# Kernel optimization log

Hardware: AMD Instinct MI355X
Metric: run time of the kernel (lower is better)

Reference implementation:

```python
import jax, jax.numpy as jnp
import numpy as np

T_SEG = 8      # n_segment
KSZ = 3        # LAM temporal kernel size
PAD = 1        # LAM temporal padding
BN_EPS = 1e-5


def setup_inputs() -> dict:
    key = jax.random.key(0)
    ks = jax.random.split(key, 12)
    n, t, c, h, w = 8, T_SEG, 256, 56, 56
    return {
        "x": jax.random.normal(ks[0], (n * t, c, h, w), jnp.float32),
        "net_w": jax.random.normal(ks[1], (c, c, 3, 3), jnp.float32) * 0.02,
        "net_b": jax.random.normal(ks[2], (c,), jnp.float32) * 0.02,
        "lam_w": jax.random.normal(ks[3], (c, c), jnp.float32) * 0.02,
        "lam_b": jax.random.normal(ks[4], (c,), jnp.float32) * 0.02,
        "mlp_w1": jax.random.normal(ks[5], (2 * t, t), jnp.float32) * 0.3,
        "bn_gamma": jax.random.uniform(ks[6], (2 * t,), jnp.float32, 0.5, 1.5),
        "bn_beta": jax.random.normal(ks[7], (2 * t,), jnp.float32) * 0.1,
        "bn_mean": jax.random.normal(ks[8], (2 * t,), jnp.float32) * 0.1,
        "bn_var": jax.random.uniform(ks[9], (2 * t,), jnp.float32, 0.5, 1.5),
        "mlp_w2": jax.random.normal(ks[10], (KSZ, 2 * t), jnp.float32) * 0.3,
        "me_w": jax.random.normal(ks[11], (3,), jnp.float32) * 0.3,
    }


def reference(x, net_w, net_b, lam_w, lam_b, mlp_w1, bn_gamma, bn_beta,
              bn_mean, bn_var, mlp_w2, me_w):
    t = T_SEG
    nt, c, h, w = x.shape
    n = nt // t

    # --- wrapped net: Conv2d 3x3, pad 1 ---
    out = jax.lax.conv_general_dilated(
        x, net_w, window_strides=(1, 1), padding="SAME",
        dimension_numbers=("NCHW", "OIHW", "NCHW"))
    out = out + net_b[None, :, None, None]

    # --- LAM ---
    new_x = out.reshape(n, t, c, h, w).transpose(0, 2, 1, 3, 4)  # (n,c,t,h,w)
    x_g = new_x.mean(axis=(2, 3, 4))                   # global pool -> (n,c)
    x_g = x_g @ lam_w.T + lam_b                        # Conv1d k=1 == matmul
    new_x = new_x + x_g[:, :, None, None, None]

    pooled = new_x.mean(axis=(3, 4)).reshape(n * c, t)  # per-(n,c) temporal sig
    hdn = pooled @ mlp_w1.T                              # (n*c, 2t), no bias
    hdn = (hdn - bn_mean) * (bn_gamma / jnp.sqrt(bn_var + BN_EPS)) + bn_beta
    hdn = jax.nn.relu(hdn)
    wgt = jax.nn.softmax(hdn @ mlp_w2.T, axis=-1).reshape(n, c, KSZ)

    # grouped conv2d (groups=n*c) == per-(n,c) depthwise temporal conv
    xpad = jnp.pad(new_x, ((0, 0), (0, 0), (PAD, PAD), (0, 0), (0, 0)))
    lam_out = sum(wgt[:, :, k, None, None, None] * xpad[:, :, k:k + t]
                  for k in range(KSZ))                  # (n,c,t,h,w)
    lam_out = lam_out.transpose(0, 2, 1, 3, 4).reshape(nt, c, h, w)

    # --- ME ---
    xv = lam_out.reshape(n, t, c, h, w)
    diff = xv[:, 1:] - xv[:, :-1]                       # frame differences
    diff = jnp.pad(diff, ((0, 0), (0, 1), (0, 0), (0, 0), (0, 0)))
    diff = diff.reshape(nt, c, h, w)
    y = diff.mean(axis=(2, 3))                          # (nt, c)
    ypad = jnp.pad(y, ((0, 0), (1, 1)))                 # conv1d over channel dim
    yc = sum(me_w[k] * ypad[:, k:k + c] for k in range(3))
    gate = jax.nn.sigmoid(yc)[:, :, None, None]

    return gate * lam_out
```

## Files before the change

kernel.cpp:

```cpp
#include <hip/hip_runtime.h>
#include <hip/hip_bf16.h>
#include <stdint.h>

#define AS1 __attribute__((address_space(1)))
#define AS3 __attribute__((address_space(3)))

typedef __attribute__((ext_vector_type(8))) short short8v;
typedef __attribute__((ext_vector_type(4))) unsigned short ushort4v;
typedef __attribute__((ext_vector_type(4))) float float4v;

#define NT 64
#define CCH 256
#define HH 56
#define WW 56
#define HWSZ 3136
#define HP 58
#define WP 58

#define OFF_XT   0ull
#define SZ_XT    110231552ull
#define OFF_WPK  (OFF_XT + SZ_XT)
#define SZ_WPK   1179648ull
#define OFF_CS   (OFF_WPK + SZ_WPK)
#define SZ_CS    65536ull
#define OFF_XG2  (OFF_CS + SZ_CS)
#define SZ_XG2   8192ull
#define OFF_WGT  (OFF_XG2 + SZ_XG2)
#define SZ_WGT   24576ull
#define OFF_GATE (OFF_WGT + SZ_WGT)
#define SZ_GATE  65536ull
#define OFF_CVT  (OFF_GATE + SZ_GATE)
#define SZ_CVT   102760448ull

__device__ __forceinline__ unsigned short f2bf(float f) {
    unsigned int u = __float_as_uint(f);
    unsigned int r = (u + 0x7fffu + ((u >> 16) & 1u)) >> 16;
    return (unsigned short)r;
}
__device__ __forceinline__ float bf2f(unsigned short u) {
    return __uint_as_float(((unsigned int)u) << 16);
}

__device__ __forceinline__ void gload16(const unsigned short* g, unsigned short* l) {
    __builtin_amdgcn_global_load_lds((const AS1 void*)g, (AS3 void*)l, 16, 0, 0);
}

__global__ __launch_bounds__(256) void k0_transpose(const float* __restrict__ x,
                                                    unsigned short* __restrict__ xt) {
    int b = blockIdx.x;
    int cb = b & 3;
    int h  = (b >> 2) % 56;
    int nt = b / (4 * 56);
    int c0 = cb * 64;
    int tid = threadIdx.x;

    __shared__ float xs[64 * 57];

    const float* src = x + ((size_t)nt * CCH + c0) * HWSZ + h * WW;
    for (int li = tid; li < 896; li += 256) {
        int row = li / 14, f4 = li % 14;
        float4v v = *(const float4v*)(src + (size_t)row * HWSZ + f4 * 4);
        float* d = &xs[row * 57 + f4 * 4];
        d[0] = v.x; d[1] = v.y; d[2] = v.z; d[3] = v.w;
    }
    __syncthreads();

    unsigned short* dst = xt + (((size_t)nt * HP + (h + 1)) * WP) * CCH + c0;
    for (int job = tid; job < 464; job += 256) {
        int ww = job >> 3, cg = job & 7;
        short8v v;
        if (ww == 0 || ww == 57) {
            v = (short8v){0,0,0,0,0,0,0,0};
        } else {
            #pragma unroll
            for (int jj = 0; jj < 8; ++jj)
                v[jj] = (short)f2bf(xs[(cg * 8 + jj) * 57 + (ww - 1)]);
        }
        *(short8v*)(dst + ww * CCH + cg * 8) = v;
    }
    if (h == 0) {
        unsigned short* d0  = xt + ((size_t)nt * HP + 0)  * WP * CCH + c0;
        unsigned short* d57 = xt + ((size_t)nt * HP + 57) * WP * CCH + c0;
        short8v z = (short8v){0,0,0,0,0,0,0,0};
        for (int job = tid; job < 464; job += 256) {
            int ww = job >> 3, cg = job & 7;
            *(short8v*)(d0  + ww * CCH + cg * 8) = z;
            *(short8v*)(d57 + ww * CCH + cg * 8) = z;
        }
    }
}

__global__ __launch_bounds__(256) void kw_pack(const float* __restrict__ nw,
                                               unsigned short* __restrict__ wpk) {
    int idx = blockIdx.x * 256 + threadIdx.x;
    int rs = idx >> 16;
    int k  = (idx >> 8) & 255;
    int c  = idx & 255;
    wpk[idx] = f2bf(nw[(k * 256 + c) * 9 + rs]);
}


#define STGALL(bi_, tA_, tB_) do { \
    gload16(wpk + (tA_) + aoffg0, &lds[(bi_) * 8192 + ldsa0]); \
    gload16(wpk + (tA_) + aoffg1, &lds[(bi_) * 8192 + ldsa1]); \
    gload16(xt  + (tB_) + boffg,  &lds[24576 + (bi_) * 4096 + ldsb]); \
} while (0)

#define LDAF(mi) (*(const short8v*)&lds[abase + (wm * 64 + (mi) * 16 + r16) * 32 + pA * 8])
#define LDBF(j)  (*(const short8v*)&lds[bbase + (wp * 64 + (j) * 16 + r16) * 32 + pA * 8])

#define BARSYNC do { \
    __builtin_amdgcn_s_barrier(); \
    __builtin_amdgcn_sched_barrier(0); \
} while (0)

template <int OB>
__global__ __launch_bounds__(512, 4) void conv_mfma(const unsigned short* __restrict__ xt,
                                                    const unsigned short* __restrict__ wpk,
                                                    const float* __restrict__ net_b,
                                                    float* __restrict__ out,
                                                    unsigned short* __restrict__ cvt,
                                                    float* __restrict__ chansum) {
    __shared__ unsigned short lds[36864];

    const int tid  = threadIdx.x;
    const int lane = tid & 63;
    const int wid  = tid >> 6;
    const int wm   = wid >> 1;
    const int wp   = wid & 1;
    const int r16  = lane & 15;
    const int hi   = lane >> 4;
    const int pA   = (hi + (r16 >> 1)) & 3;

    const int pb0 = (blockIdx.x & 7) * 192 + (blockIdx.x >> 3);

    const int cgs = ((tid & 3) - (tid >> 3)) & 3;
    const int aoffg0 = (tid >> 2) * 256 + cgs * 8;
    const int aoffg1 = aoffg0 + 32768;
    const int ldsa0  = tid * 8;
    const int ldsa1  = ldsa0 + 4096;
    const int ldsb   = tid * 8;

    for (int g = pb0; g < 1568; g += 1536) {
        const int p0 = g * 128;

        long boffg;
        {
            int r = tid >> 2;
            int p = p0 + r;
            int nt = p / HWSZ, hw = p - nt * HWSZ;
            int hh = hw / WW,  w  = hw - hh * WW;
            boffg = ((long)(nt * HP + hh) * WP + w) * 256 + cgs * 8;
        }

        float4v acc[4][4];
        #pragma unroll
        for (int i = 0; i < 4; ++i)
            #pragma unroll
            for (int j = 0; j < 4; ++j) acc[i][j] = (float4v){0.f, 0.f, 0.f, 0.f};

        STGALL(0, 0, 0);
        STGALL(1, 32, 32);

        int cur = 0;
        for (int kt = 0; kt < 72; ++kt) {
            const int abase = cur * 8192;
            const int bbase = 24576 + cur * 4096;

            if (kt < 70) {
                const int ktn = kt + 2;
                int nb2 = cur + 2; if (nb2 >= 3) nb2 -= 3;
                const int rsn = ktn >> 3, con = (ktn & 7) * 32;
                const int tAn = rsn * 65536 + con;
                const int tBn = ((rsn / 3) * WP + (rsn - (rsn / 3) * 3)) * 256 + con;
                STGALL(nb2, tAn, tBn);
                asm volatile("s_waitcnt vmcnt(6)" ::: "memory");
            } else if (kt == 70) {
                asm volatile("s_waitcnt vmcnt(3)" ::: "memory");
            } else {
                asm volatile("s_waitcnt vmcnt(0)" ::: "memory");
            }
            BARSYNC;

            short8v afrag[4], bfrag[4];
            #pragma unroll
            for (int mi = 0; mi < 4; ++mi) afrag[mi] = LDAF(mi);
            #pragma unroll
            for (int j = 0; j < 4; ++j) bfrag[j] = LDBF(j);

            asm volatile("s_waitcnt lgkmcnt(0)" ::: "memory");
            __builtin_amdgcn_sched_barrier(0);
            __builtin_amdgcn_s_setprio(1);
            #pragma unroll
            for (int j = 0; j < 4; ++j)
                #pragma unroll
                for (int mi = 0; mi < 4; ++mi)
                    acc[mi][j] = __builtin_amdgcn_mfma_f32_16x16x32_bf16(afrag[mi], bfrag[j], acc[mi][j], 0, 0, 0);
            __builtin_amdgcn_s_setprio(0);
            BARSYNC;

            ++cur; if (cur >= 3) cur = 0;
        }

        const int pw = p0 + wp * 64;
        const int ntw = pw / HWSZ;
        const int hwb = pw - ntw * HWSZ;
        #pragma unroll
        for (int mi = 0; mi < 4; ++mi) {
            #pragma unroll
            for (int r = 0; r < 4; ++r) {
                const int m = wm * 64 + mi * 16 + hi * 4 + r;
                const float bias = net_b[m];
                float csum = 0.f;
                const size_t obase = ((size_t)ntw * CCH + m) * HWSZ + hwb;
                #pragma unroll
                for (int j = 0; j < 4; ++j) {
                    float v = acc[mi][j][r] + bias;
                    if (OB) cvt[obase + j * 16 + r16] = f2bf(v);
                    else    out[obase + j * 16 + r16] = v;
                    csum += v;
                }
                csum += __shfl_xor(csum, 1);
                csum += __shfl_xor(csum, 2);
                csum += __shfl_xor(csum, 4);
                csum += __shfl_xor(csum, 8);
                if (r16 == 0) atomicAdd(&chansum[ntw * CCH + m], csum);
            }
        }
    }
}

__global__ __launch_bounds__(256) void k234(const float* __restrict__ chansum,
                                            const float* __restrict__ lam_w,
                                            const float* __restrict__ lam_b,
                                            const float* __restrict__ mw1,
                                            const float* __restrict__ bg,
                                            const float* __restrict__ bb,
                                            const float* __restrict__ bm,
                                            const float* __restrict__ bv,
                                            const float* __restrict__ mw2,
                                            const float* __restrict__ me_w,
                                            float* __restrict__ xg2,
                                            float* __restrict__ wgt,
                                            float* __restrict__ gate) {
    int n = blockIdx.x, c = threadIdx.x;
    __shared__ float xs[256];
    __shared__ float yd[8][256];

    float s = 0.f;
    #pragma unroll
    for (int t = 0; t < 8; ++t) s += chansum[(n * 8 + t) * CCH + c];
    xs[c] = s * (1.0f / (3136.f * 8.f));
    __syncthreads();

    float xg = lam_b[c];
    const float* row = lam_w + c * 256;
    for (int cc = 0; cc < 256; ++cc) xg += row[cc] * xs[cc];
    xg2[n * 256 + c] = xg;

    float p[8];
    #pragma unroll
    for (int t = 0; t < 8; ++t)
        p[t] = chansum[(n * 8 + t) * CCH + c] * (1.0f / 3136.f) + xg;

    float hd[16];
    #pragma unroll
    for (int j = 0; j < 16; ++j) {
        float v = 0.f;
        #pragma unroll
        for (int t = 0; t < 8; ++t) v += p[t] * mw1[j * 8 + t];
        v = (v - bm[j]) * (bg[j] * rsqrtf(bv[j] + 1e-5f)) + bb[j];
        hd[j] = fmaxf(v, 0.f);
    }
    float lg[3];
    #pragma unroll
    for (int k = 0; k < 3; ++k) {
        float v = 0.f;
        #pragma unroll
        for (int j = 0; j < 16; ++j) v += hd[j] * mw2[k * 16 + j];
        lg[k] = v;
    }
    float mx = fmaxf(fmaxf(lg[0], lg[1]), lg[2]);
    float e0 = expf(lg[0] - mx), e1 = expf(lg[1] - mx), e2 = expf(lg[2] - mx);
    float inv = 1.f / (e0 + e1 + e2);
    float wk[3] = {e0 * inv, e1 * inv, e2 * inv};
    int idx = n * 256 + c;
    #pragma unroll
    for (int k = 0; k < 3; ++k) wgt[idx * 3 + k] = wk[k];

    float mb[8];
    #pragma unroll
    for (int t = 0; t < 8; ++t) {
        float v = 0.f;
        #pragma unroll
        for (int k = 0; k < 3; ++k) {
            int tt = t + k - 1;
            if (tt >= 0 && tt < 8) v += wk[k] * p[tt];
        }
        mb[t] = v;
    }
    #pragma unroll
    for (int t = 0; t < 7; ++t) yd[t][c] = mb[t + 1] - mb[t];
    yd[7][c] = 0.f;
    __syncthreads();

    float w0 = me_w[0], w1v = me_w[1], w2v = me_w[2];
    #pragma unroll
    for (int t = 0; t < 8; ++t) {
        float yc = w1v * yd[t][c];
        if (c > 0)   yc += w0 * yd[t][c - 1];
        if (c < 255) yc += w2v * yd[t][c + 1];
        gate[(n * 8 + t) * CCH + c] = 1.f / (1.f + expf(-yc));
    }
}

template <int OB>
__global__ __launch_bounds__(256) void k5_final(float* __restrict__ out,
                                                const unsigned short* __restrict__ cvt,
                                                const float* __restrict__ wgt,
                                                const float* __restrict__ xg2,
                                                const float* __restrict__ gate) {
    int tid = blockIdx.x * 256 + threadIdx.x;
    int hw4 = tid % 784;
    int nc = tid / 784;
    int n = nc >> 8, c = nc & 255;
    float w0 = wgt[nc * 3 + 0], w1 = wgt[nc * 3 + 1], w2 = wgt[nc * 3 + 2];
    float xg = xg2[nc];
    const size_t tstride = (size_t)CCH * HWSZ;
    size_t base = ((size_t)(n * 8) * CCH + c) * HWSZ + hw4 * 4;

    float4v o[8];
    #pragma unroll
    for (int t = 0; t < 8; ++t) {
        if (OB) {
            ushort4v v = *(const ushort4v*)(cvt + base + t * tstride);
            #pragma unroll
            for (int q = 0; q < 4; ++q) o[t][q] = bf2f(v[q]);
        } else {
            o[t] = *(const float4v*)(out + base + t * tstride);
        }
    }

    #pragma unroll
    for (int t = 0; t < 8; ++t) {
        float g = gate[(n * 8 + t) * CCH + c];
        float4v lam;
        #pragma unroll
        for (int q = 0; q < 4; ++q) {
            float v = w1 * (o[t][q] + xg);
            if (t > 0) v += w0 * (o[t - 1][q] + xg);
            if (t < 7) v += w2 * (o[t + 1][q] + xg);
            lam[q] = g * v;
        }
        *(float4v*)(out + base + t * tstride) = lam;
    }
}

extern "C" void kernel_launch(void* const* d_in, const int* in_sizes, int n_in,
                              void* d_out, int out_size, void* d_ws, size_t ws_size,
                              hipStream_t stream) {
    const float* x      = (const float*)d_in[0];
    const float* net_w  = (const float*)d_in[1];
    const float* net_b  = (const float*)d_in[2];
    const float* lam_w  = (const float*)d_in[3];
    const float* lam_b  = (const float*)d_in[4];
    const float* mlp_w1 = (const float*)d_in[5];
    const float* bn_g   = (const float*)d_in[6];
    const float* bn_b   = (const float*)d_in[7];
    const float* bn_m   = (const float*)d_in[8];
    const float* bn_v   = (const float*)d_in[9];
    const float* mlp_w2 = (const float*)d_in[10];
    const float* me_w   = (const float*)d_in[11];
    float* out = (float*)d_out;

    char* ws = (char*)d_ws;
    unsigned short* xt  = (unsigned short*)(ws + OFF_XT);
    unsigned short* wpk = (unsigned short*)(ws + OFF_WPK);
    float* chansum = (float*)(ws + OFF_CS);
    float* xg2     = (float*)(ws + OFF_XG2);
    float* wgt     = (float*)(ws + OFF_WGT);
    float* gate    = (float*)(ws + OFF_GATE);
    unsigned short* cvt = (unsigned short*)(ws + OFF_CVT);

    const bool use_bf16 = (ws_size >= OFF_CVT + SZ_CVT);

    hipMemsetAsync(chansum, 0, SZ_CS, stream);
    kw_pack<<<2304, 256, 0, stream>>>(net_w, wpk);
    k0_transpose<<<64 * 56 * 4, 256, 0, stream>>>(x, xt);
    if (use_bf16)
        conv_mfma<1><<<1536, 512, 0, stream>>>(xt, wpk, net_b, out, cvt, chansum);
    else
        conv_mfma<0><<<1536, 512, 0, stream>>>(xt, wpk, net_b, out, cvt, chansum);
    k234<<<8, 256, 0, stream>>>(chansum, lam_w, lam_b, mlp_w1, bn_g, bn_b, bn_m, bn_v,
                                mlp_w2, me_w, xg2, wgt, gate);
    if (use_bf16)
        k5_final<1><<<6272, 256, 0, stream>>>(out, cvt, wgt, xg2, gate);
    else
        k5_final<0><<<6272, 256, 0, stream>>>(out, cvt, wgt, xg2, gate);
}
```

Baseline: 412.5 us.

## Split tail conv tiles along K across extra blocks with atomic accumulation

The conv GEMM has 1568 pixel tiles but launched 1536 blocks, so 32 blocks ran a second full tile serially, creating a long tail. The tail 32 tiles are now split into two K-halves each, handled by 64 extra blocks that atomically add partial results into a bias-preinitialized fp32 output. A new init kernel writes the bias into the tail region and the bias contribution into the channel sums, and the final kernel reads tail pixels from fp32 instead of bf16. This adds an extra kernel launch and float atomics on the output in exchange for removing the serialized second wave.

```diff
diff --git a/kernel.cpp b/kernel.cpp
--- a/kernel.cpp
+++ b/kernel.cpp
@@ -16,6 +16,7 @@
 #define HWSZ 3136
 #define HP 58
 #define WP 58
+#define TAILP 196608
 
 #define OFF_XT   0ull
 #define SZ_XT    110231552ull
@@ -99,6 +100,23 @@
     wpk[idx] = f2bf(nw[(k * 256 + c) * 9 + rs]);
 }
 
+__global__ __launch_bounds__(256) void kinit(const float* __restrict__ net_b,
+                                             float* __restrict__ out,
+                                             float* __restrict__ chansum) {
+    int idx = blockIdx.x * 256 + threadIdx.x;
+    int m  = idx >> 12;
+    int pp = idx & 4095;
+    int p  = TAILP + pp;
+    int nt = p / HWSZ, hw = p - nt * HWSZ;
+    out[((size_t)nt * CCH + m) * HWSZ + hw] = net_b[m];
+    if (pp < 512) {
+        int img = 62 + (pp >> 8);
+        int mm  = pp & 255;
+        float npix = (img == 62) ? 960.f : 3136.f;
+        chansum[img * CCH + mm] = npix * net_b[mm];
+    }
+}
+
 
 #define STGALL(bi_, tA_, tB_) do { \
     gload16(wpk + (tA_) + aoffg0, &lds[(bi_) * 8192 + ldsa0]); \
@@ -109,10 +127,30 @@
 #define LDAF(mi) (*(const short8v*)&lds[abase + (wm * 64 + (mi) * 16 + r16) * 32 + pA * 8])
 #define LDBF(j)  (*(const short8v*)&lds[bbase + (wp * 64 + (j) * 16 + r16) * 32 + pA * 8])
 
+#define KTA(kt) ((((kt) >> 3) << 16) + (((kt) & 7) * 32))
+#define KTB(kt) (((((kt) >> 3) / 3) * WP + (((kt) >> 3) - (((kt) >> 3) / 3) * 3)) * 256 + (((kt) & 7) * 32))
+
 #define BARSYNC do { \
     __builtin_amdgcn_s_barrier(); \
     __builtin_amdgcn_sched_barrier(0); \
 } while (0)
+
+#define KTILE_BODY \
+    short8v afrag[4], bfrag[4]; \
+    _Pragma("unroll") \
+    for (int mi = 0; mi < 4; ++mi) afrag[mi] = LDAF(mi); \
+    _Pragma("unroll") \
+    for (int j = 0; j < 4; ++j) bfrag[j] = LDBF(j); \
+    asm volatile("s_waitcnt lgkmcnt(0)" ::: "memory"); \
+    __builtin_amdgcn_sched_barrier(0); \
+    __builtin_amdgcn_s_setprio(1); \
+    _Pragma("unroll") \
+    for (int j = 0; j < 4; ++j) \
+        _Pragma("unroll") \
+        for (int mi = 0; mi < 4; ++mi) \
+            acc[mi][j] = __builtin_amdgcn_mfma_f32_16x16x32_bf16(afrag[mi], bfrag[j], acc[mi][j], 0, 0, 0); \
+    __builtin_amdgcn_s_setprio(0); \
+    BARSYNC;
 
 template <int OB>
 __global__ __launch_bounds__(512, 4) void conv_mfma(const unsigned short* __restrict__ xt,
@@ -132,7 +170,7 @@
     const int hi   = lane >> 4;
     const int pA   = (hi + (r16 >> 1)) & 3;
 
-    const int pb0 = (blockIdx.x & 7) * 192 + (blockIdx.x >> 3);
+    const int bid = blockIdx.x;
 
     const int cgs = ((tid & 3) - (tid >> 3)) & 3;
     const int aoffg0 = (tid >> 2) * 256 + cgs * 8;
@@ -141,8 +179,15 @@
     const int ldsa1  = ldsa0 + 4096;
     const int ldsb   = tid * 8;
 
-    for (int g = pb0; g < 1568; g += 1536) {
-        const int p0 = g * 128;
+    float4v acc[4][4];
+    #pragma unroll
+    for (int i = 0; i < 4; ++i)
+        #pragma unroll
+        for (int j = 0; j < 4; ++j) acc[i][j] = (float4v){0.f, 0.f, 0.f, 0.f};
+
+    if (bid < 1536) {
+        const int pb0 = (bid & 7) * 192 + (bid >> 3);
+        const int p0 = pb0 * 128;
 
         long boffg;
         {
@@ -153,12 +198,6 @@
             boffg = ((long)(nt * HP + hh) * WP + w) * 256 + cgs * 8;
         }
 
-        float4v acc[4][4];
-        #pragma unroll
-        for (int i = 0; i < 4; ++i)
-            #pragma unroll
-            for (int j = 0; j < 4; ++j) acc[i][j] = (float4v){0.f, 0.f, 0.f, 0.f};
-
         STGALL(0, 0, 0);
         STGALL(1, 32, 32);
 
@@ -170,10 +209,7 @@
             if (kt < 70) {
                 const int ktn = kt + 2;
                 int nb2 = cur + 2; if (nb2 >= 3) nb2 -= 3;
-                const int rsn = ktn >> 3, con = (ktn & 7) * 32;
-                const int tAn = rsn * 65536 + con;
-                const int tBn = ((rsn / 3) * WP + (rsn - (rsn / 3) * 3)) * 256 + con;
-                STGALL(nb2, tAn, tBn);
+                STGALL(nb2, KTA(ktn), KTB(ktn));
                 asm volatile("s_waitcnt vmcnt(6)" ::: "memory");
             } else if (kt == 70) {
                 asm volatile("s_waitcnt vmcnt(3)" ::: "memory");
@@ -182,23 +218,7 @@
             }
             BARSYNC;
 
-            short8v afrag[4], bfrag[4];
-            #pragma unroll
-            for (int mi = 0; mi < 4; ++mi) afrag[mi] = LDAF(mi);
-            #pragma unroll
-            for (int j = 0; j < 4; ++j) bfrag[j] = LDBF(j);
-
-            asm volatile("s_waitcnt lgkmcnt(0)" ::: "memory");
-            __builtin_amdgcn_sched_barrier(0);
-            __builtin_amdgcn_s_setprio(1);
-            #pragma unroll
-            for (int j = 0; j < 4; ++j)
-                #pragma unroll
-                for (int mi = 0; mi < 4; ++mi)
-                    acc[mi][j] = __builtin_amdgcn_mfma_f32_16x16x32_bf16(afrag[mi], bfrag[j], acc[mi][j], 0, 0, 0);
-            __builtin_amdgcn_s_setprio(0);
-            BARSYNC;
-
+            KTILE_BODY
             ++cur; if (cur >= 3) cur = 0;
         }
 
@@ -227,6 +247,67 @@
                 if (r16 == 0) atomicAdd(&chansum[ntw * CCH + m], csum);
             }
         }
+    } else {
+        const int tb = bid - 1536;
+        const int p0 = (1536 + (tb >> 1)) * 128;
+        const int k0 = (tb & 1) * 36;
+
+        long boffg;
+        {
+            int r = tid >> 2;
+            int p = p0 + r;
+            int nt = p / HWSZ, hw = p - nt * HWSZ;
+            int hh = hw / WW,  w  = hw - hh * WW;
+            boffg = ((long)(nt * HP + hh) * WP + w) * 256 + cgs * 8;
+        }
+
+        STGALL(0, KTA(k0), KTB(k0));
+        STGALL(1, KTA(k0 + 1), KTB(k0 + 1));
+
+        int cur = 0;
+        for (int i = 0; i < 36; ++i) {
+            const int abase = cur * 8192;
+            const int bbase = 24576 + cur * 4096;
+
+            if (i < 34) {
+                int nb2 = cur + 2; if (nb2 >= 3) nb2 -= 3;
+                const int ktn = k0 + i + 2;
+                STGALL(nb2, KTA(ktn), KTB(ktn));
+                asm volatile("s_waitcnt vmcnt(6)" ::: "memory");
+            } else if (i == 34) {
+                asm volatile("s_waitcnt vmcnt(3)" ::: "memory");
+            } else {
+                asm volatile("s_waitcnt vmcnt(0)" ::: "memory");
+            }
+            BARSYNC;
+
+            KTILE_BODY
+            ++cur; if (cur >= 3) cur = 0;
+        }
+
+        const int pw = p0 + wp * 64;
+        const int ntw = pw / HWSZ;
+        const int hwb = pw - ntw * HWSZ;
+        #pragma unroll
+        for (int mi = 0; mi < 4; ++mi) {
+            #pragma unroll
+            for (int r = 0; r < 4; ++r) {
+                const int m = wm * 64 + mi * 16 + hi * 4 + r;
+                float csum = 0.f;
+                float* orow = out + ((size_t)ntw * CCH + m) * HWSZ + hwb;
+                #pragma unroll
+                for (int j = 0; j < 4; ++j) {
+                    float v = acc[mi][j][r];
+                    atomicAdd(&orow[j * 16 + r16], v);
+                    csum += v;
+                }
+                csum += __shfl_xor(csum, 1);
+                csum += __shfl_xor(csum, 2);
+                csum += __shfl_xor(csum, 4);
+                csum += __shfl_xor(csum, 8);
+                if (r16 == 0) atomicAdd(&chansum[ntw * CCH + m], csum);
+            }
+        }
     }
 }
 
@@ -332,12 +413,18 @@
     float4v o[8];
     #pragma unroll
     for (int t = 0; t < 8; ++t) {
+        size_t addr = base + t * tstride;
         if (OB) {
-            ushort4v v = *(const ushort4v*)(cvt + base + t * tstride);
-            #pragma unroll
-            for (int q = 0; q < 4; ++q) o[t][q] = bf2f(v[q]);
+            int p = (n * 8 + t) * HWSZ + hw4 * 4;
+            if (p >= TAILP) {
+                o[t] = *(const float4v*)(out + addr);
+            } else {
+                ushort4v v = *(const ushort4v*)(cvt + addr);
+                #pragma unroll
+                for (int q = 0; q < 4; ++q) o[t][q] = bf2f(v[q]);
+            }
         } else {
-            o[t] = *(const float4v*)(out + base + t * tstride);
+            o[t] = *(const float4v*)(out + addr);
         }
     }
 
@@ -386,11 +473,12 @@
 
     hipMemsetAsync(chansum, 0, SZ_CS, stream);
     kw_pack<<<2304, 256, 0, stream>>>(net_w, wpk);
+    kinit<<<4096, 256, 0, stream>>>(net_b, out, chansum);
     k0_transpose<<<64 * 56 * 4, 256, 0, stream>>>(x, xt);
     if (use_bf16)
-        conv_mfma<1><<<1536, 512, 0, stream>>>(xt, wpk, net_b, out, cvt, chansum);
+        conv_mfma<1><<<1600, 512, 0, stream>>>(xt, wpk, net_b, out, cvt, chansum);
     else
-        conv_mfma<0><<<1536, 512, 0, stream>>>(xt, wpk, net_b, out, cvt, chansum);
+        conv_mfma<0><<<1600, 512, 0, stream>>>(xt, wpk, net_b, out, cvt, chansum);
     k234<<<8, 256, 0, stream>>>(chansum, lam_w, lam_b, mlp_w1, bn_g, bn_b, bn_m, bn_v,
                                 mlp_w2, me_w, xg2, wgt, gate);
     if (use_bf16)
```

Result: no change. 405.1 us, median of 2 (-1.8%).
